# Performance work log

Hardware: AMD Instinct MI355X
Metric: run time of the kernel (lower is better)

Reference implementation:

```python
import jax, jax.numpy as jnp
import numpy as np

NUM_ITERATIONS = 3


def _squash(s):
    # s: [B, J, S]. Faithful to the torch code: squash norm is computed over
    # dim=2 of s_j [B,1,J,S,1], i.e. the num_unit (J) axis here.
    mag_sq = jnp.sum(s * s, axis=1, keepdims=True)  # [B, 1, S]
    mag = jnp.sqrt(mag_sq)
    return s * (mag_sq / (1.0 + mag_sq) / mag)


def setup_inputs() -> dict:
    key = jax.random.key(0)
    k1, k2 = jax.random.split(key)
    B, U, C, J, S = 128, 8, 2048, 32, 16
    x = jax.random.normal(k1, (B, U, C), dtype=jnp.float32)
    W = jax.random.normal(k2, (1, C, J, S, U), dtype=jnp.float32)
    return {"x": x, "W": W}


def reference(x, W):
    # x: [B, in_unit, in_channel]; W: [1, C, J, S, U]
    xt = jnp.swapaxes(x, 1, 2)          # [B, C, U]
    Wc = W[0]                           # [C, J, S, U]
    # u_hat = W @ x (per input capsule c, output capsule j): [B, C, J, S]
    u_hat = jnp.einsum('cjsu,bcu->bcjs', Wc, xt)
    B, C, J, _ = u_hat.shape
    b = jnp.zeros((C, J), dtype=u_hat.dtype)
    v = None
    for _ in range(NUM_ITERATIONS):
        # legacy F.softmax on 4D [1,C,J,1] defaults to dim=1 -> over C
        c = jax.nn.softmax(b, axis=0)                      # [C, J]
        s = jnp.einsum('cj,bcjs->bjs', c, u_hat)           # [B, J, S]
        v = _squash(s)                                     # [B, J, S]
        # agreement, mean over batch (keepdim handled by shape [C,J])
        b = b + jnp.einsum('bcjs,bjs->cj', u_hat, v) / B
    return v[..., None]  # [B, num_unit, unit_size, 1] == v_j.squeeze(1)
```

## Files before the change

### kernel.cpp

```cpp
#include <hip/hip_runtime.h>
#include <hip/hip_bf16.h>

#define BB 128
#define UU 8
#define CC 2048
#define JJ 32
#define SS 16

typedef unsigned int u32;
typedef unsigned short u16;
typedef __attribute__((ext_vector_type(8))) short bf16x8;
typedef __attribute__((ext_vector_type(4))) float f32x4;

__device__ __forceinline__ float bflo(u32 p) { return __uint_as_float(p << 16); }
__device__ __forceinline__ float bfhi(u32 p) { return __uint_as_float(p & 0xffff0000u); }
__device__ __forceinline__ u32 f2b(float f) {
    u32 bits = __float_as_uint(f);
    u32 r = bits + 0x7fffu + ((bits >> 16) & 1u);
    return r >> 16;
}
__device__ __forceinline__ u32 pack2(float a, float b) { return f2b(a) | (f2b(b) << 16); }

__global__ __launch_bounds__(256) void k_setup(const u32* __restrict__ x,
                                               const u32* __restrict__ W,
                                               int* __restrict__ flags,
                                               float* __restrict__ bbp) {
    int blk = blockIdx.x, t = threadIdx.x;
    if (blk < 2) {
        __shared__ int red[4];
        const u32* p = blk ? W : x;
        int cnt = 0;
        for (int i = t; i < 2048; i += 256) {
            u32 e = (p[i] >> 7) & 0xFF;
            cnt += (e >= 0x60 && e <= 0x8F) ? 1 : 0;
        }
#pragma unroll
        for (int o = 32; o > 0; o >>= 1) cnt += __shfl_down(cnt, o, 64);
        if ((t & 63) == 0) red[t >> 6] = cnt;
        __syncthreads();
        if (t == 0) flags[blk] = ((red[0] + red[1] + red[2] + red[3]) > 1228) ? 1 : 0;
    } else {
        int base = (blk - 2) * 4096 + t;
#pragma unroll
        for (int r = 0; r < 16; ++r) bbp[base + r * 256] = 0.f;
    }
}

__global__ __launch_bounds__(256) void k_build_xA(const void* __restrict__ x,
                                                  u16* __restrict__ xA,
                                                  const int* __restrict__ flag) {
    int b = blockIdx.x >> 3;
    int c = (blockIdx.x & 7) * 256 + threadIdx.x;
    uint4 p;
    if (*flag) {
        const u16* xh = (const u16*)x + (size_t)b * UU * CC;
        u16 v[8];
#pragma unroll
        for (int u = 0; u < 8; ++u) v[u] = xh[u * CC + c];
        p.x = (u32)v[0] | ((u32)v[1] << 16);
        p.y = (u32)v[2] | ((u32)v[3] << 16);
        p.z = (u32)v[4] | ((u32)v[5] << 16);
        p.w = (u32)v[6] | ((u32)v[7] << 16);
    } else {
        const float* xf = (const float*)x + (size_t)b * UU * CC;
        float v[8];
#pragma unroll
        for (int u = 0; u < 8; ++u) v[u] = xf[u * CC + c];
        p.x = pack2(v[0], v[1]);
        p.y = pack2(v[2], v[3]);
        p.z = pack2(v[4], v[5]);
        p.w = pack2(v[6], v[7]);
    }
    ((uint4*)xA)[(size_t)b * CC + c] = p;
}

__global__ __launch_bounds__(256) void k_build_xB(const void* __restrict__ x,
                                                  u16* __restrict__ xB,
                                                  const int* __restrict__ flag) {
    __shared__ float lds[16][129];
    int u = blockIdx.x >> 7;
    int c0 = (blockIdx.x & 127) * 16;
    int t = threadIdx.x;
    int b = t >> 1, h = t & 1;
    size_t row = ((size_t)b * UU + u) * CC + c0;
    if (*flag) {
        const u16* xh = (const u16*)x + row + h * 8;
#pragma unroll
        for (int e = 0; e < 8; ++e) lds[h * 8 + e][b] = bflo((u32)xh[e]);
    } else {
        const float4* x4 = (const float4*)((const float*)x + row);
        float4 lo = x4[h * 2], hi = x4[h * 2 + 1];
        lds[h * 8 + 0][b] = lo.x; lds[h * 8 + 1][b] = lo.y;
        lds[h * 8 + 2][b] = lo.z; lds[h * 8 + 3][b] = lo.w;
        lds[h * 8 + 4][b] = hi.x; lds[h * 8 + 5][b] = hi.y;
        lds[h * 8 + 6][b] = hi.z; lds[h * 8 + 7][b] = hi.w;
    }
    __syncthreads();
    int ci = t >> 4, k8 = t & 15;
    uint4 p;
    p.x = pack2(lds[ci][k8 * 8 + 0], lds[ci][k8 * 8 + 1]);
    p.y = pack2(lds[ci][k8 * 8 + 2], lds[ci][k8 * 8 + 3]);
    p.z = pack2(lds[ci][k8 * 8 + 4], lds[ci][k8 * 8 + 5]);
    p.w = pack2(lds[ci][k8 * 8 + 6], lds[ci][k8 * 8 + 7]);
    ((uint4*)xB)[((size_t)u * CC + c0 + ci) * 16 + k8] = p;
}

__global__ __launch_bounds__(256) void k_build_Wn(const void* __restrict__ W,
                                                  u16* __restrict__ Wn,
                                                  const int* __restrict__ flag) {
    __shared__ uint4 lds[16][129];
    int ct = blockIdx.x & 127, nt = blockIdx.x >> 7;
    int c0 = ct * 16, n0 = nt * 128;
    int t = threadIdx.x;
    int isbf = *flag;
    for (int q = t; q < 2048; q += 256) {
        int ci = q >> 7, ni = q & 127;
        size_t widx = (size_t)(c0 + ci) * 512 + n0 + ni;
        uint4 o;
        if (isbf) {
            o = ((const uint4*)W)[widx];
        } else {
            const float4* Wf = (const float4*)W;
            float4 lo = Wf[2 * widx], hi = Wf[2 * widx + 1];
            o.x = pack2(lo.x, lo.y);
            o.y = pack2(lo.z, lo.w);
            o.z = pack2(hi.x, hi.y);
            o.w = pack2(hi.z, hi.w);
        }
        lds[ci][ni] = o;
    }
    __syncthreads();
    for (int q = t; q < 2048; q += 256) {
        int ni = q >> 4, ci = q & 15;
        ((uint4*)Wn)[(size_t)(n0 + ni) * 2048 + c0 + ci] = lds[ci][ni];
    }
}

__global__ __launch_bounds__(256) void k_softmax(const float* __restrict__ bbp,
                                                 float* __restrict__ ccp) {
    int j = blockIdx.x, t = threadIdx.x;
    __shared__ float red[4];
    __shared__ float bcast[2];
    const float* row = bbp + j * CC;
    float m = -1e30f;
    for (int c = t; c < CC; c += 256) m = fmaxf(m, row[c]);
#pragma unroll
    for (int o = 32; o > 0; o >>= 1) m = fmaxf(m, __shfl_down(m, o, 64));
    if ((t & 63) == 0) red[t >> 6] = m;
    __syncthreads();
    if (t == 0) bcast[0] = fmaxf(fmaxf(red[0], red[1]), fmaxf(red[2], red[3]));
    __syncthreads();
    float mm = bcast[0];
    float ssum = 0.f;
    for (int c = t; c < CC; c += 256) ssum += expf(row[c] - mm);
#pragma unroll
    for (int o = 32; o > 0; o >>= 1) ssum += __shfl_down(ssum, o, 64);
    if ((t & 63) == 0) red[t >> 6] = ssum;
    __syncthreads();
    if (t == 0) bcast[1] = red[0] + red[1] + red[2] + red[3];
    __syncthreads();
    float inv = 1.0f / bcast[1];
    for (int c = t; c < CC; c += 256) ccp[j * CC + c] = expf(row[c] - mm) * inv;
}

__global__ __launch_bounds__(256) void k_bmatlite(const u16* __restrict__ Wn,
                                                  const float* __restrict__ ccp,
                                                  u16* __restrict__ Bm) {
    int g = blockIdx.x * 256 + threadIdx.x;
    int n = g >> 11, c = g & 2047;
    uint4 p = ((const uint4*)Wn)[g];
    float cw = ccp[(n >> 4) * CC + c];
    uint4 o;
    o.x = pack2(bflo(p.x) * cw, bfhi(p.x) * cw);
    o.y = pack2(bflo(p.y) * cw, bfhi(p.y) * cw);
    o.z = pack2(bflo(p.z) * cw, bfhi(p.z) * cw);
    o.w = pack2(bflo(p.w) * cw, bfhi(p.w) * cw);
    ((uint4*)Bm)[g] = o;
}

__global__ __launch_bounds__(256) void k_gemmA(const u16* __restrict__ xA,
                                               const u16* __restrict__ Bmat,
                                               float* __restrict__ spart) {
    const bf16x8* A8 = (const bf16x8*)xA;
    const bf16x8* B8 = (const bf16x8*)Bmat;
    int t = threadIdx.x;
    int w = t >> 6, lane = t & 63;
    int gw = blockIdx.x * 4 + w;
    int sl = gw >> 6, rest = gw & 63;
    int mg = rest & 3, ng = rest >> 2;
    int ln = lane & 15, quad = lane >> 4;
    int rowA0 = (mg * 32 + ln) * 2048;
    int rowA1 = rowA0 + 16 * 2048;
    int rowB0 = (ng * 32 + ln) * 2048;
    int rowB1 = rowB0 + 16 * 2048;
    int kk = sl * 64 + quad;
    f32x4 acc00 = {0.f, 0.f, 0.f, 0.f};
    f32x4 acc01 = acc00, acc10 = acc00, acc11 = acc00;
#pragma unroll 4
    for (int step = 0; step < 16; ++step) {
        bf16x8 a0 = A8[rowA0 + kk];
        bf16x8 a1 = A8[rowA1 + kk];
        bf16x8 b0 = B8[rowB0 + kk];
        bf16x8 b1 = B8[rowB1 + kk];
        kk += 4;
        acc00 = __builtin_amdgcn_mfma_f32_16x16x32_bf16(a0, b0, acc00, 0, 0, 0);
        acc01 = __builtin_amdgcn_mfma_f32_16x16x32_bf16(a0, b1, acc01, 0, 0, 0);
        acc10 = __builtin_amdgcn_mfma_f32_16x16x32_bf16(a1, b0, acc10, 0, 0, 0);
        acc11 = __builtin_amdgcn_mfma_f32_16x16x32_bf16(a1, b1, acc11, 0, 0, 0);
    }
    float* outp = spart + sl * (BB * JJ * SS);
    int b0r = mg * 32 + quad * 4;
    int n00 = ng * 32 + ln;
#pragma unroll
    for (int r = 0; r < 4; ++r) {
        int b = b0r + r;
        outp[b * 512 + n00] = acc00[r];
        outp[b * 512 + n00 + 16] = acc01[r];
        outp[(b + 16) * 512 + n00] = acc10[r];
        outp[(b + 16) * 512 + n00 + 16] = acc11[r];
    }
}

__global__ __launch_bounds__(512) void k_rsq(const float* __restrict__ spart,
                                             u16* __restrict__ vB,
                                             float* __restrict__ out,
                                             float scale_pre, int write_out) {
    __shared__ float s[512];
    __shared__ float sc[16];
    int b = blockIdx.x, n = threadIdx.x;
    float v = 0.f;
#pragma unroll
    for (int sl = 0; sl < 32; ++sl) v += spart[sl * (BB * JJ * SS) + b * 512 + n];
    v *= scale_pre;
    s[n] = v;
    __syncthreads();
    if (n < 16) {
        float msq = 0.f;
#pragma unroll
        for (int jj = 0; jj < 32; ++jj) {
            float t = s[jj * 16 + n];
            msq = fmaf(t, t, msq);
        }
        sc[n] = msq / ((1.f + msq) * sqrtf(fmaxf(msq, 1e-30f)));
    }
    __syncthreads();
    float vv = s[n] * sc[n & 15];
    vB[n * BB + b] = (u16)f2b(vv);
    if (write_out) out[b * 512 + n] = vv;
}

__global__ __launch_bounds__(256) void k_gemmB1(const u16* __restrict__ vB,
                                                const u16* __restrict__ xB,
                                                u16* __restrict__ G) {
    const bf16x8* A8 = (const bf16x8*)vB;
    const bf16x8* B8 = (const bf16x8*)xB;
    int t = threadIdx.x;
    int w = t >> 6, lane = t & 63;
    int gw = blockIdx.x * 4 + w;
    int u = gw >> 10, rest = gw & 1023;
    int n0 = (rest & 15) * 32, c0 = (rest >> 4) * 32;
    int ln = lane & 15, quad = lane >> 4;
    bf16x8 av[2][4], bx[2][4];
#pragma unroll
    for (int mt = 0; mt < 2; ++mt)
#pragma unroll
        for (int st = 0; st < 4; ++st)
            av[mt][st] = A8[(n0 + mt * 16 + ln) * 16 + quad + 4 * st];
#pragma unroll
    for (int ct = 0; ct < 2; ++ct)
#pragma unroll
        for (int st = 0; st < 4; ++st)
            bx[ct][st] = B8[((size_t)u * CC + c0 + ct * 16 + ln) * 16 + quad + 4 * st];
    f32x4 acc[2][2];
    acc[0][0] = {0.f, 0.f, 0.f, 0.f};
    acc[0][1] = acc[0][0]; acc[1][0] = acc[0][0]; acc[1][1] = acc[0][0];
#pragma unroll
    for (int st = 0; st < 4; ++st)
#pragma unroll
        for (int mt = 0; mt < 2; ++mt)
#pragma unroll
            for (int ct = 0; ct < 2; ++ct)
                acc[mt][ct] = __builtin_amdgcn_mfma_f32_16x16x32_bf16(
                    av[mt][st], bx[ct][st], acc[mt][ct], 0, 0, 0);
#pragma unroll
    for (int mt = 0; mt < 2; ++mt)
#pragma unroll
        for (int ct = 0; ct < 2; ++ct)
#pragma unroll
            for (int r = 0; r < 4; ++r) {
                int n = n0 + mt * 16 + quad * 4 + r;
                int c = c0 + ct * 16 + ln;
                G[((size_t)u * 512 + n) * 2048 + c] = (u16)f2b(acc[mt][ct][r]);
            }
}

__global__ __launch_bounds__(256) void k_bbsum(const void* __restrict__ W,
                                               const u16* __restrict__ G,
                                               float* __restrict__ bbp,
                                               const int* __restrict__ wflag) {
    __shared__ u32 Wlds[128][33];
    __shared__ float red[4][128];
    int j = blockIdx.x & 31;
    int c0 = ((blockIdx.x >> 5) & 15) * 128;
    int sh = blockIdx.x >> 9;
    int t = threadIdx.x;
    int isbf = *wflag;
#pragma unroll
    for (int it = 0; it < 8; ++it) {
        int q = t + it * 256;
        int ci = q >> 4, f4 = q & 15;
        size_t fbase = ((size_t)(c0 + ci) * 512 + j * 16 + sh * 8) * 8 + f4 * 4;
        u32 p0, p1;
        if (isbf) {
            const u32* W32 = (const u32*)W;
            p0 = W32[fbase >> 1];
            p1 = W32[(fbase >> 1) + 1];
        } else {
            float4 f = ((const float4*)W)[fbase >> 2];
            p0 = pack2(f.x, f.y);
            p1 = pack2(f.z, f.w);
        }
        Wlds[ci][f4 * 2] = p0;
        Wlds[ci][f4 * 2 + 1] = p1;
    }
    __syncthreads();
    int w = t >> 6, cp = t & 63;
    const u32* G32 = (const u32*)G;
    float acc0 = 0.f, acc1 = 0.f;
    int u0 = 2 * w;
#pragma unroll
    for (int s = 0; s < 8; ++s) {
        u32 wl = Wlds[2 * cp][s * 4 + w];
        u32 wh = Wlds[2 * cp + 1][s * 4 + w];
        int n = j * 16 + sh * 8 + s;
        u32 g0 = G32[((size_t)u0 * 512 + n) * 1024 + (c0 >> 1) + cp];
        u32 g1 = G32[((size_t)(u0 + 1) * 512 + n) * 1024 + (c0 >> 1) + cp];
        acc0 = fmaf(bflo(wl), bflo(g0), acc0);
        acc0 = fmaf(bfhi(wl), bflo(g1), acc0);
        acc1 = fmaf(bflo(wh), bfhi(g0), acc1);
        acc1 = fmaf(bfhi(wh), bfhi(g1), acc1);
    }
    red[w][2 * cp] = acc0;
    red[w][2 * cp + 1] = acc1;
    __syncthreads();
    if (t < 128) {
        float sum = red[0][t] + red[1][t] + red[2][t] + red[3][t];
        atomicAdd(&bbp[j * CC + c0 + t], sum * (1.0f / BB));
    }
}

extern "C" void kernel_launch(void* const* d_in, const int* in_sizes, int n_in,
                              void* d_out, int out_size, void* d_ws, size_t ws_size,
                              hipStream_t stream) {
    const void* x = d_in[0];
    const void* W = d_in[1];
    if (in_sizes[0] == CC * JJ * SS * UU) {
        x = d_in[1];
        W = d_in[0];
    }
    float* out = (float*)d_out;

    char* ws = (char*)d_ws;
    u16* Bm = (u16*)ws;
    u16* G = (u16*)ws;
    u16* xA = (u16*)(ws + (16u << 20));
    u16* xB = (u16*)(ws + (20u << 20));
    u16* Wn = (u16*)(ws + (24u << 20));
    float* spart = (float*)(ws + (40u << 20));
    size_t b48 = (size_t)48u << 20;
    u16* vB = (u16*)(ws + b48);
    float* bbp = (float*)(ws + b48 + 131072);
    float* ccp = (float*)(ws + b48 + 393216);
    int* flags = (int*)(ws + b48 + 655360);

    k_setup<<<18, 256, 0, stream>>>((const u32*)x, (const u32*)W, flags, bbp);
    k_build_xA<<<1024, 256, 0, stream>>>(x, xA, flags + 0);
    k_build_xB<<<1024, 256, 0, stream>>>(x, xB, flags + 0);
    k_build_Wn<<<512, 256, 0, stream>>>(W, Wn, flags + 1);

    for (int it = 0; it < 3; ++it) {
        const u16* Bsrc = Wn;
        float scale_pre = 1.0f / 2048.0f;
        if (it > 0) {
            k_softmax<<<32, 256, 0, stream>>>(bbp, ccp);
            k_bmatlite<<<4096, 256, 0, stream>>>(Wn, ccp, Bm);
            Bsrc = Bm;
            scale_pre = 1.0f;
        }
        k_gemmA<<<512, 256, 0, stream>>>(xA, Bsrc, spart);
        k_rsq<<<128, 512, 0, stream>>>(spart, vB, out, scale_pre, it == 2 ? 1 : 0);
        if (it < 2) {
            k_gemmB1<<<2048, 256, 0, stream>>>(vB, xB, G);
            k_bbsum<<<1024, 256, 0, stream>>>(W, G, bbp, flags + 1);
        }
    }
}
```

Baseline: 244.2 us.

## Fuse prep kernels, fold softmax coupling scaling into GEMM, reuse bf16 W

The setup, xA, xB and Wn build kernels are merged into one k_prep launch. The runtime bf16/fp32 input detection flags are dropped and fp32 inputs are assumed. The separate k_bmatlite pass that wrote a coupling-scaled copy of W is removed; k_gemmA now scales the bf16 W tiles by the softmax coefficients inline. k_bbsum now reads the pre-converted bf16 Wn instead of reconverting fp32 W. Together these cut launches and a full write-plus-read of a large scaled-weight buffer, at the cost of extra ALU work in the GEMM inner loop.

```diff
diff --git a/kernel.cpp b/kernel.cpp
--- a/kernel.cpp
+++ b/kernel.cpp
@@ -20,119 +20,81 @@
     return r >> 16;
 }
 __device__ __forceinline__ u32 pack2(float a, float b) { return f2b(a) | (f2b(b) << 16); }
-
-__global__ __launch_bounds__(256) void k_setup(const u32* __restrict__ x,
-                                               const u32* __restrict__ W,
-                                               int* __restrict__ flags,
-                                               float* __restrict__ bbp) {
+__device__ __forceinline__ uint4 scale4(uint4 p, float cw) {
+    uint4 o;
+    o.x = pack2(bflo(p.x) * cw, bfhi(p.x) * cw);
+    o.y = pack2(bflo(p.y) * cw, bfhi(p.y) * cw);
+    o.z = pack2(bflo(p.z) * cw, bfhi(p.z) * cw);
+    o.w = pack2(bflo(p.w) * cw, bfhi(p.w) * cw);
+    return o;
+}
+
+__global__ __launch_bounds__(256) void k_prep(const float* __restrict__ x,
+                                              const float* __restrict__ W,
+                                              u16* __restrict__ xA,
+                                              u16* __restrict__ xB,
+                                              u16* __restrict__ Wn,
+                                              float* __restrict__ bbp) {
+    __shared__ uint4 ldsu[16][129];
     int blk = blockIdx.x, t = threadIdx.x;
-    if (blk < 2) {
-        __shared__ int red[4];
-        const u32* p = blk ? W : x;
-        int cnt = 0;
-        for (int i = t; i < 2048; i += 256) {
-            u32 e = (p[i] >> 7) & 0xFF;
-            cnt += (e >= 0x60 && e <= 0x8F) ? 1 : 0;
-        }
-#pragma unroll
-        for (int o = 32; o > 0; o >>= 1) cnt += __shfl_down(cnt, o, 64);
-        if ((t & 63) == 0) red[t >> 6] = cnt;
-        __syncthreads();
-        if (t == 0) flags[blk] = ((red[0] + red[1] + red[2] + red[3]) > 1228) ? 1 : 0;
-    } else {
-        int base = (blk - 2) * 4096 + t;
-#pragma unroll
-        for (int r = 0; r < 16; ++r) bbp[base + r * 256] = 0.f;
-    }
-}
-
-__global__ __launch_bounds__(256) void k_build_xA(const void* __restrict__ x,
-                                                  u16* __restrict__ xA,
-                                                  const int* __restrict__ flag) {
-    int b = blockIdx.x >> 3;
-    int c = (blockIdx.x & 7) * 256 + threadIdx.x;
-    uint4 p;
-    if (*flag) {
-        const u16* xh = (const u16*)x + (size_t)b * UU * CC;
-        u16 v[8];
-#pragma unroll
-        for (int u = 0; u < 8; ++u) v[u] = xh[u * CC + c];
-        p.x = (u32)v[0] | ((u32)v[1] << 16);
-        p.y = (u32)v[2] | ((u32)v[3] << 16);
-        p.z = (u32)v[4] | ((u32)v[5] << 16);
-        p.w = (u32)v[6] | ((u32)v[7] << 16);
-    } else {
-        const float* xf = (const float*)x + (size_t)b * UU * CC;
+    if (blk < 1024) {
+        int b = blk >> 3;
+        int c = (blk & 7) * 256 + t;
+        const float* xf = x + (size_t)b * UU * CC;
         float v[8];
 #pragma unroll
         for (int u = 0; u < 8; ++u) v[u] = xf[u * CC + c];
+        uint4 p;
         p.x = pack2(v[0], v[1]);
         p.y = pack2(v[2], v[3]);
         p.z = pack2(v[4], v[5]);
         p.w = pack2(v[6], v[7]);
-    }
-    ((uint4*)xA)[(size_t)b * CC + c] = p;
-}
-
-__global__ __launch_bounds__(256) void k_build_xB(const void* __restrict__ x,
-                                                  u16* __restrict__ xB,
-                                                  const int* __restrict__ flag) {
-    __shared__ float lds[16][129];
-    int u = blockIdx.x >> 7;
-    int c0 = (blockIdx.x & 127) * 16;
-    int t = threadIdx.x;
-    int b = t >> 1, h = t & 1;
-    size_t row = ((size_t)b * UU + u) * CC + c0;
-    if (*flag) {
-        const u16* xh = (const u16*)x + row + h * 8;
-#pragma unroll
-        for (int e = 0; e < 8; ++e) lds[h * 8 + e][b] = bflo((u32)xh[e]);
-    } else {
-        const float4* x4 = (const float4*)((const float*)x + row);
+        ((uint4*)xA)[(size_t)b * CC + c] = p;
+    } else if (blk < 2048) {
+        int bb2 = blk - 1024;
+        int u = bb2 >> 7, c0 = (bb2 & 127) * 16;
+        float* ldsf = (float*)ldsu;
+        int b = t >> 1, h = t & 1;
+        const float4* x4 = (const float4*)(x + ((size_t)b * UU + u) * CC + c0);
         float4 lo = x4[h * 2], hi = x4[h * 2 + 1];
-        lds[h * 8 + 0][b] = lo.x; lds[h * 8 + 1][b] = lo.y;
-        lds[h * 8 + 2][b] = lo.z; lds[h * 8 + 3][b] = lo.w;
-        lds[h * 8 + 4][b] = hi.x; lds[h * 8 + 5][b] = hi.y;
-        lds[h * 8 + 6][b] = hi.z; lds[h * 8 + 7][b] = hi.w;
-    }
-    __syncthreads();
-    int ci = t >> 4, k8 = t & 15;
-    uint4 p;
-    p.x = pack2(lds[ci][k8 * 8 + 0], lds[ci][k8 * 8 + 1]);
-    p.y = pack2(lds[ci][k8 * 8 + 2], lds[ci][k8 * 8 + 3]);
-    p.z = pack2(lds[ci][k8 * 8 + 4], lds[ci][k8 * 8 + 5]);
-    p.w = pack2(lds[ci][k8 * 8 + 6], lds[ci][k8 * 8 + 7]);
-    ((uint4*)xB)[((size_t)u * CC + c0 + ci) * 16 + k8] = p;
-}
-
-__global__ __launch_bounds__(256) void k_build_Wn(const void* __restrict__ W,
-                                                  u16* __restrict__ Wn,
-                                                  const int* __restrict__ flag) {
-    __shared__ uint4 lds[16][129];
-    int ct = blockIdx.x & 127, nt = blockIdx.x >> 7;
-    int c0 = ct * 16, n0 = nt * 128;
-    int t = threadIdx.x;
-    int isbf = *flag;
-    for (int q = t; q < 2048; q += 256) {
-        int ci = q >> 7, ni = q & 127;
-        size_t widx = (size_t)(c0 + ci) * 512 + n0 + ni;
-        uint4 o;
-        if (isbf) {
-            o = ((const uint4*)W)[widx];
-        } else {
-            const float4* Wf = (const float4*)W;
+        ldsf[(h * 8 + 0) * 129 + b] = lo.x; ldsf[(h * 8 + 1) * 129 + b] = lo.y;
+        ldsf[(h * 8 + 2) * 129 + b] = lo.z; ldsf[(h * 8 + 3) * 129 + b] = lo.w;
+        ldsf[(h * 8 + 4) * 129 + b] = hi.x; ldsf[(h * 8 + 5) * 129 + b] = hi.y;
+        ldsf[(h * 8 + 6) * 129 + b] = hi.z; ldsf[(h * 8 + 7) * 129 + b] = hi.w;
+        __syncthreads();
+        int ci = t >> 4, k8 = t & 15;
+        const float* r = ldsf + ci * 129 + k8 * 8;
+        uint4 p;
+        p.x = pack2(r[0], r[1]);
+        p.y = pack2(r[2], r[3]);
+        p.z = pack2(r[4], r[5]);
+        p.w = pack2(r[6], r[7]);
+        ((uint4*)xB)[((size_t)u * CC + c0 + ci) * 16 + k8] = p;
+    } else if (blk < 2560) {
+        int bb2 = blk - 2048;
+        int ct = bb2 & 127, nt = bb2 >> 7;
+        int c0 = ct * 16, n0 = nt * 128;
+        const float4* Wf = (const float4*)W;
+        for (int q = t; q < 2048; q += 256) {
+            int ci = q >> 7, ni = q & 127;
+            size_t widx = (size_t)(c0 + ci) * 512 + n0 + ni;
             float4 lo = Wf[2 * widx], hi = Wf[2 * widx + 1];
+            uint4 o;
             o.x = pack2(lo.x, lo.y);
             o.y = pack2(lo.z, lo.w);
             o.z = pack2(hi.x, hi.y);
             o.w = pack2(hi.z, hi.w);
-        }
-        lds[ci][ni] = o;
-    }
-    __syncthreads();
-    for (int q = t; q < 2048; q += 256) {
-        int ni = q >> 4, ci = q & 15;
-        ((uint4*)Wn)[(size_t)(n0 + ni) * 2048 + c0 + ci] = lds[ci][ni];
+            ldsu[ci][ni] = o;
+        }
+        __syncthreads();
+        for (int q = t; q < 2048; q += 256) {
+            int ni = q >> 4, ci = q & 15;
+            ((uint4*)Wn)[(size_t)(n0 + ni) * 2048 + c0 + ci] = ldsu[ci][ni];
+        }
+    } else {
+        int base = (blk - 2560) * 4096 + t;
+#pragma unroll
+        for (int r = 0; r < 16; ++r) bbp[base + r * 256] = 0.f;
     }
 }
 
@@ -163,26 +125,13 @@
     for (int c = t; c < CC; c += 256) ccp[j * CC + c] = expf(row[c] - mm) * inv;
 }
 
-__global__ __launch_bounds__(256) void k_bmatlite(const u16* __restrict__ Wn,
-                                                  const float* __restrict__ ccp,
-                                                  u16* __restrict__ Bm) {
-    int g = blockIdx.x * 256 + threadIdx.x;
-    int n = g >> 11, c = g & 2047;
-    uint4 p = ((const uint4*)Wn)[g];
-    float cw = ccp[(n >> 4) * CC + c];
-    uint4 o;
-    o.x = pack2(bflo(p.x) * cw, bfhi(p.x) * cw);
-    o.y = pack2(bflo(p.y) * cw, bfhi(p.y) * cw);
-    o.z = pack2(bflo(p.z) * cw, bfhi(p.z) * cw);
-    o.w = pack2(bflo(p.w) * cw, bfhi(p.w) * cw);
-    ((uint4*)Bm)[g] = o;
-}
-
 __global__ __launch_bounds__(256) void k_gemmA(const u16* __restrict__ xA,
-                                               const u16* __restrict__ Bmat,
+                                               const u16* __restrict__ Wn,
+                                               const float* __restrict__ ccp,
+                                               int use_cc,
                                                float* __restrict__ spart) {
     const bf16x8* A8 = (const bf16x8*)xA;
-    const bf16x8* B8 = (const bf16x8*)Bmat;
+    const uint4* B4 = (const uint4*)Wn;
     int t = threadIdx.x;
     int w = t >> 6, lane = t & 63;
     int gw = blockIdx.x * 4 + w;
@@ -193,6 +142,8 @@
     int rowA1 = rowA0 + 16 * 2048;
     int rowB0 = (ng * 32 + ln) * 2048;
     int rowB1 = rowB0 + 16 * 2048;
+    const float* cc0 = ccp + (2 * ng) * CC;
+    const float* cc1 = cc0 + CC;
     int kk = sl * 64 + quad;
     f32x4 acc00 = {0.f, 0.f, 0.f, 0.f};
     f32x4 acc01 = acc00, acc10 = acc00, acc11 = acc00;
@@ -200,8 +151,16 @@
     for (int step = 0; step < 16; ++step) {
         bf16x8 a0 = A8[rowA0 + kk];
         bf16x8 a1 = A8[rowA1 + kk];
-        bf16x8 b0 = B8[rowB0 + kk];
-        bf16x8 b1 = B8[rowB1 + kk];
+        uint4 wb0 = B4[rowB0 + kk];
+        uint4 wb1 = B4[rowB1 + kk];
+        if (use_cc) {
+            float cw0 = cc0[kk];
+            float cw1 = cc1[kk];
+            wb0 = scale4(wb0, cw0);
+            wb1 = scale4(wb1, cw1);
+        }
+        bf16x8 b0 = __builtin_bit_cast(bf16x8, wb0);
+        bf16x8 b1 = __builtin_bit_cast(bf16x8, wb1);
         kk += 4;
         acc00 = __builtin_amdgcn_mfma_f32_16x16x32_bf16(a0, b0, acc00, 0, 0, 0);
         acc01 = __builtin_amdgcn_mfma_f32_16x16x32_bf16(a0, b1, acc01, 0, 0, 0);
@@ -238,8 +197,8 @@
         float msq = 0.f;
 #pragma unroll
         for (int jj = 0; jj < 32; ++jj) {
-            float t = s[jj * 16 + n];
-            msq = fmaf(t, t, msq);
+            float tv = s[jj * 16 + n];
+            msq = fmaf(tv, tv, msq);
         }
         sc[n] = msq / ((1.f + msq) * sqrtf(fmaxf(msq, 1e-30f)));
     }
@@ -294,34 +253,25 @@
             }
 }
 
-__global__ __launch_bounds__(256) void k_bbsum(const void* __restrict__ W,
+__global__ __launch_bounds__(256) void k_bbsum(const u16* __restrict__ Wn,
                                                const u16* __restrict__ G,
-                                               float* __restrict__ bbp,
-                                               const int* __restrict__ wflag) {
+                                               float* __restrict__ bbp) {
     __shared__ u32 Wlds[128][33];
     __shared__ float red[4][128];
     int j = blockIdx.x & 31;
     int c0 = ((blockIdx.x >> 5) & 15) * 128;
     int sh = blockIdx.x >> 9;
     int t = threadIdx.x;
-    int isbf = *wflag;
-#pragma unroll
-    for (int it = 0; it < 8; ++it) {
+    const uint4* Wn4 = (const uint4*)Wn;
+#pragma unroll
+    for (int it = 0; it < 4; ++it) {
         int q = t + it * 256;
-        int ci = q >> 4, f4 = q & 15;
-        size_t fbase = ((size_t)(c0 + ci) * 512 + j * 16 + sh * 8) * 8 + f4 * 4;
-        u32 p0, p1;
-        if (isbf) {
-            const u32* W32 = (const u32*)W;
-            p0 = W32[fbase >> 1];
-            p1 = W32[(fbase >> 1) + 1];
-        } else {
-            float4 f = ((const float4*)W)[fbase >> 2];
-            p0 = pack2(f.x, f.y);
-            p1 = pack2(f.z, f.w);
-        }
-        Wlds[ci][f4 * 2] = p0;
-        Wlds[ci][f4 * 2 + 1] = p1;
+        int ci = q & 127, s = q >> 7;
+        uint4 p = Wn4[(size_t)(j * 16 + sh * 8 + s) * 2048 + c0 + ci];
+        Wlds[ci][s * 4 + 0] = p.x;
+        Wlds[ci][s * 4 + 1] = p.y;
+        Wlds[ci][s * 4 + 2] = p.z;
+        Wlds[ci][s * 4 + 3] = p.w;
     }
     __syncthreads();
     int w = t >> 6, cp = t & 63;
@@ -352,16 +302,15 @@
 extern "C" void kernel_launch(void* const* d_in, const int* in_sizes, int n_in,
                               void* d_out, int out_size, void* d_ws, size_t ws_size,
                               hipStream_t stream) {
-    const void* x = d_in[0];
-    const void* W = d_in[1];
+    const float* x = (const float*)d_in[0];
+    const float* W = (const float*)d_in[1];
     if (in_sizes[0] == CC * JJ * SS * UU) {
-        x = d_in[1];
-        W = d_in[0];
+        x = (const float*)d_in[1];
+        W = (const float*)d_in[0];
     }
     float* out = (float*)d_out;
 
     char* ws = (char*)d_ws;
-    u16* Bm = (u16*)ws;
     u16* G = (u16*)ws;
     u16* xA = (u16*)(ws + (16u << 20));
     u16* xB = (u16*)(ws + (20u << 20));
@@ -371,27 +320,18 @@
     u16* vB = (u16*)(ws + b48);
     float* bbp = (float*)(ws + b48 + 131072);
     float* ccp = (float*)(ws + b48 + 393216);
-    int* flags = (int*)(ws + b48 + 655360);
-
-    k_setup<<<18, 256, 0, stream>>>((const u32*)x, (const u32*)W, flags, bbp);
-    k_build_xA<<<1024, 256, 0, stream>>>(x, xA, flags + 0);
-    k_build_xB<<<1024, 256, 0, stream>>>(x, xB, flags + 0);
-    k_build_Wn<<<512, 256, 0, stream>>>(W, Wn, flags + 1);
+
+    k_prep<<<2576, 256, 0, stream>>>(x, W, xA, xB, Wn, bbp);
 
     for (int it = 0; it < 3; ++it) {
-        const u16* Bsrc = Wn;
-        float scale_pre = 1.0f / 2048.0f;
-        if (it > 0) {
-            k_softmax<<<32, 256, 0, stream>>>(bbp, ccp);
-            k_bmatlite<<<4096, 256, 0, stream>>>(Wn, ccp, Bm);
-            Bsrc = Bm;
-            scale_pre = 1.0f;
-        }
-        k_gemmA<<<512, 256, 0, stream>>>(xA, Bsrc, spart);
-        k_rsq<<<128, 512, 0, stream>>>(spart, vB, out, scale_pre, it == 2 ? 1 : 0);
+        if (it > 0) k_softmax<<<32, 256, 0, stream>>>(bbp, ccp);
+        k_gemmA<<<512, 256, 0, stream>>>(xA, Wn, ccp, it > 0 ? 1 : 0, spart);
+        k_rsq<<<128, 512, 0, stream>>>(spart, vB, out,
+                                       it == 0 ? (1.0f / 2048.0f) : 1.0f,
+                                       it == 2 ? 1 : 0);
         if (it < 2) {
             k_gemmB1<<<2048, 256, 0, stream>>>(vB, xB, G);
-            k_bbsum<<<1024, 256, 0, stream>>>(W, G, bbp, flags + 1);
-        }
-    }
-}
+            k_bbsum<<<1024, 256, 0, stream>>>(Wn, G, bbp);
+        }
+    }
+}
```

Measured after the change: 215.4 us. 11.8% less time.
